# Performance work log

Hardware: AMD Instinct MI355X
Metric: run time of the kernel (lower is better)

The kernel has to match this reference:

```python
import jax, jax.numpy as jnp
import numpy as np

T, H, W, B = 9, 128, 128, 8  # size=[9,128,128], 8 samples in batch
N = 4194304


def _avg3(x):
    # AvgPool3d(kernel=(1,3,3), stride=1, pad=(0,1,1), count_include_pad=True)
    s = jax.lax.reduce_window(x, 0.0, jax.lax.add, (1, 1, 1, 3, 3), (1, 1, 1, 1, 1),
                              ((0, 0), (0, 0), (0, 0), (1, 1), (1, 1)))
    return s / 9.0


def _inorm(x, eps=1e-5):
    # InstanceNorm3d(affine=False): normalize over (T,H,W) per sample/channel
    m = x.mean(axis=(2, 3, 4), keepdims=True)
    v = x.var(axis=(2, 3, 4), keepdims=True)
    return (x - m) * jax.lax.rsqrt(v + eps)


def _time_corr(x):
    bx = (x > 0).astype(x.dtype)
    bx = jnp.concatenate([bx, bx[:, :, -1:]], axis=2)  # ReplicationPad3d back in T
    prev = _avg3(bx)
    around = (prev[:, :, :-1] * bx[:, :, 1:] > 4.0 / 9.0).astype(x.dtype)
    return _avg3(around)


def _dyn_conv(x, fc1_w, fc2_w, dyn_w):
    # Dynamic_Conv, kernel (3,1,1): attention over k=4 weight banks, per-sample conv
    a = x.mean(axis=(2, 3, 4))                       # [B,C] global avg pool
    a = jax.nn.relu(a @ fc1_w.T)
    a = jax.nn.softmax(a @ fc2_w.T, axis=1)          # [B,k]
    w = jnp.einsum('bk,koid->boid', a, dyn_w)        # [B,O,I,3]
    xp = jnp.pad(x, ((0, 0), (0, 0), (1, 1), (0, 0), (0, 0)))  # pad T
    t = x.shape[2]
    out = jnp.einsum('boi,bithw->bothw', w[..., 0], xp[:, :, 0:t])
    out = out + jnp.einsum('boi,bithw->bothw', w[..., 1], xp[:, :, 1:1 + t])
    out = out + jnp.einsum('boi,bithw->bothw', w[..., 2], xp[:, :, 2:2 + t])
    return out


def _voxelize(t, x, y, p, b):
    # per-batch normalize t by max, then bilinear-in-time scatter-add over T bins
    tmax = jax.ops.segment_max(t, b, num_segments=B)
    ts = (t / tmax[b]) * T                                         # [N]
    bins = jnp.arange(T, dtype=ts.dtype)
    vals = jnp.maximum(1.0 - jnp.abs(ts[None, :] - bins[:, None]), 0.0)  # [T,N]
    base = x + W * y + W * H * T * p + 2 * W * H * T * b           # [N]
    idx = base[None, :] + W * H * jnp.arange(T, dtype=base.dtype)[:, None]
    vox = jnp.zeros(B * 2 * T * H * W, dtype=ts.dtype).at[idx].add(vals)
    return vox.reshape(B, 2, T, H, W)


def setup_inputs() -> dict:
    key = jax.random.key(0)
    ks = jax.random.split(key, 10)
    t = jax.random.uniform(ks[0], (N,), dtype=jnp.float32)
    x = jax.random.randint(ks[1], (N,), 0, W, dtype=jnp.int32)
    y = jax.random.randint(ks[2], (N,), 0, H, dtype=jnp.int32)
    p = jax.random.randint(ks[3], (N,), 0, 2, dtype=jnp.int32)
    b = jnp.sort(jax.random.randint(ks[4], (N,), 0, B, dtype=jnp.int32))
    conv1_w = jax.random.normal(ks[5], (16, 2), jnp.float32) / np.sqrt(2.0)
    fc1_w = jax.random.normal(ks[6], (8, 16), jnp.float32) / np.sqrt(16.0)
    fc2_w = jax.random.normal(ks[7], (4, 8), jnp.float32) / np.sqrt(8.0)
    dyn_w = jax.random.normal(ks[8], (4, 16, 16, 3), jnp.float32) / np.sqrt(48.0)
    conv3_w = jax.random.normal(ks[9], (2, 16), jnp.float32) / np.sqrt(16.0)
    return {"t": t, "x": x, "y": y, "p": p, "b": b,
            "conv1_w": conv1_w, "fc1_w": fc1_w, "fc2_w": fc2_w,
            "dyn_w": dyn_w, "conv3_w": conv3_w}


def reference(t, x, y, p, b, conv1_w, fc1_w, fc2_w, dyn_w, conv3_w):
    vox = _voxelize(t, x, y, p, b)                     # [B,2,T,H,W]
    mask = _time_corr(vox)
    h = _inorm(vox)
    h = jnp.einsum('oc,bcthw->bothw', conv1_w, h)      # 1x1x1 conv 2->16
    h = _dyn_conv(h, fc1_w, fc2_w, dyn_w)
    h = jnp.einsum('oc,bcthw->bothw', conv3_w, h)      # 1x1x1 conv 16->2
    out = _inorm(jax.nn.sigmoid(h) * mask)
    return out
```

## Files before the change

### kernel.cpp

```cpp
#include <hip/hip_runtime.h>
#include <math.h>

#define TT 9
#define HH 128
#define WW 128
#define BB 8
#define SLICE (HH*WW)
#define CHW (TT*SLICE)
#define BCH (2*CHW)
#define TOT (BB*BCH)
#define INV_M (1.0f/147456.0f)
#define NYG 32
#define NBK (9*NYG)
#define SEGCAP 4096u
#define SSCALE 274877906944.0f
#define INV_SSCALE (1.0/274877906944.0)

__global__ void __launch_bounds__(1024) k_bounds(
        const int* __restrict__ b, int* __restrict__ start, int n,
        const float* __restrict__ conv1_w, const float* __restrict__ dyn_w,
        const float* __restrict__ conv3_w, float* __restrict__ Kc,
        unsigned* __restrict__ tailz, unsigned* __restrict__ cursor, int initCur) {
    if (blockIdx.x == 1) {
        if (threadIdx.x < 72) tailz[threadIdx.x] = 0u;
        if (initCur)
            for (int i = threadIdx.x; i < 8 * NBK; i += 1024)
                cursor[i] = (unsigned)i * SEGCAP;
        return;
    }
    int tid = threadIdx.x;
    if (tid < 9) {
        if (tid == 0) start[0] = 0;
        else if (tid == 8) start[8] = n;
        else {
            int lo = 0, hi = n;
            while (lo < hi) { int mid = (lo + hi) >> 1; if (b[mid] < tid) lo = mid + 1; else hi = mid; }
            start[tid] = lo;
        }
    }
    if (tid >= 32 && tid < 44) {
        int q = tid - 32;
        int d = q % 3, c = (q / 3) & 1, o2 = q / 6;
        float acc = 0.0f;
        for (int o = 0; o < 16; ++o) {
            float c3 = conv3_w[o2 * 16 + o];
            for (int i = 0; i < 16; ++i) {
                float wsum = 0.0f;
                for (int k = 0; k < 4; ++k) wsum += dyn_w[((k * 16 + o) * 16 + i) * 3 + d];
                acc += c3 * (0.25f * wsum) * conv1_w[i * 2 + c];
            }
        }
        Kc[q] = acc;
    }
}

__global__ void __launch_bounds__(1024) k_tmax(
        const float* __restrict__ t, const int* __restrict__ start,
        unsigned* __restrict__ gmax) {
    __shared__ unsigned sm[1024];
    int bi = blockIdx.x & 7, cj = blockIdx.x >> 3, nb = gridDim.x >> 3;
    int s = start[bi], e = start[bi + 1];
    unsigned m = 0u;
    if (e > s) {
        int a = (s + 3) & ~3; if (a > e) a = e;
        int z = e & ~3;       if (z < a) z = a;
        if (cj == 0) {
            int i = s + (int)threadIdx.x;
            if (i < a) { unsigned v = __float_as_uint(t[i]); if (v > m) m = v; }
            i = z + (int)threadIdx.x;
            if (i < e) { unsigned v = __float_as_uint(t[i]); if (v > m) m = v; }
        }
        long nq = (long)(z - a) >> 2;
        long per = (nq + nb - 1) / nb;
        long q0 = (long)cj * per; if (q0 > nq) q0 = nq;
        long q1 = q0 + per;       if (q1 > nq) q1 = nq;
        const float4* tp = (const float4*)(t + a);
        for (long i = q0 + threadIdx.x; i < q1; i += 1024) {
            float4 u = tp[i];
            unsigned c = __float_as_uint(fmaxf(fmaxf(u.x, u.y), fmaxf(u.z, u.w)));
            if (c > m) m = c;
        }
    }
    sm[threadIdx.x] = m;
    __syncthreads();
    for (int ofs = 512; ofs > 0; ofs >>= 1) {
        if (threadIdx.x < ofs && sm[threadIdx.x + ofs] > sm[threadIdx.x])
            sm[threadIdx.x] = sm[threadIdx.x + ofs];
        __syncthreads();
    }
    if (threadIdx.x == 0 && sm[0]) atomicMax(&gmax[bi], sm[0]);
}

__global__ void __launch_bounds__(1024) k_place(
        const float* __restrict__ t, const int* __restrict__ x,
        const int* __restrict__ y, const int* __restrict__ p,
        const unsigned* __restrict__ gmax, const int* __restrict__ start,
        unsigned* __restrict__ cursor, int2* __restrict__ rec) {
    __shared__ unsigned lh[NBK], lc[NBK], cbase[NBK];
    __shared__ unsigned wsum[5];
    __shared__ int2 srec[4096];
    __shared__ unsigned short sbkt[4096];
    int bi = blockIdx.x & 7, cj = blockIdx.x >> 3, nb = gridDim.x >> 3;
    int s = start[bi], e = start[bi + 1];
    if (e <= s) return;
    float tmax = __uint_as_float(gmax[bi]);
    int a = (s + 3) & ~3; if (a > e) a = e;
    int z = e & ~3;       if (z < a) z = a;
    long nq = (long)(z - a) >> 2;
    long per = (nq + nb - 1) / nb;
    long q0 = (long)cj * per; if (q0 > nq) q0 = nq;
    long q1 = q0 + per;       if (q1 > nq) q1 = nq;
    const float4* tp = (const float4*)(t + a);
    const int4*   xp = (const int4*)(x + a);
    const int4*   yp = (const int4*)(y + a);
    const int4*   pp = (const int4*)(p + a);
    for (long base = q0; base < q1; base += 1024) {
        if (threadIdx.x < NBK) lh[threadIdx.x] = 0u;
        __syncthreads();
        long qi = base + threadIdx.x;
        int lb[4]; float tsv[4]; int keyv[4]; unsigned rank[4];
        #pragma unroll
        for (int k = 0; k < 4; ++k) lb[k] = -1;
        if (qi < q1) {
            float4 tv = tp[qi]; int4 xv = xp[qi]; int4 yv = yp[qi]; int4 pv = pp[qi];
            float tq[4] = {tv.x, tv.y, tv.z, tv.w};
            int   xq[4] = {xv.x, xv.y, xv.z, xv.w};
            int   yq[4] = {yv.x, yv.y, yv.z, yv.w};
            int   pq[4] = {pv.x, pv.y, pv.z, pv.w};
            #pragma unroll
            for (int k = 0; k < 4; ++k) {
                float ts = tq[k] / tmax * 9.0f;
                int i0 = (int)floorf(ts);
                if ((unsigned)i0 < 9u) {
                    lb[k] = i0 * NYG + (yq[k] >> 2);
                    tsv[k] = ts;
                    keyv[k] = xq[k] + (yq[k] << 7) + (pq[k] << 14);
                }
            }
        }
        #pragma unroll
        for (int k = 0; k < 4; ++k)
            if (lb[k] >= 0) rank[k] = atomicAdd(&lh[lb[k]], 1u);
        __syncthreads();
        unsigned v = 0, inc = 0;
        if (threadIdx.x < 320) {
            v = (threadIdx.x < NBK) ? lh[threadIdx.x] : 0u;
            inc = v;
            #pragma unroll
            for (int ofs = 1; ofs < 64; ofs <<= 1) {
                unsigned u = __shfl_up(inc, ofs, 64);
                if ((threadIdx.x & 63) >= ofs) inc += u;
            }
            if ((threadIdx.x & 63) == 63) wsum[threadIdx.x >> 6] = inc;
        }
        __syncthreads();
        if (threadIdx.x < NBK) {
            unsigned ex = inc - v;
            int w = threadIdx.x >> 6;
            for (int j = 0; j < w; ++j) ex += wsum[j];
            cbase[threadIdx.x] = ex;
            lc[threadIdx.x] = v ? atomicAdd(&cursor[bi * NBK + threadIdx.x], v) : 0u;
        }
        __syncthreads();
        #pragma unroll
        for (int k = 0; k < 4; ++k)
            if (lb[k] >= 0) {
                unsigned sl_ = cbase[lb[k]] + rank[k];
                srec[sl_] = make_int2(__float_as_int(tsv[k]), keyv[k]);
                sbkt[sl_] = (unsigned short)lb[k];
            }
        __syncthreads();
        unsigned tot = cbase[NBK - 1] + lh[NBK - 1];
        #pragma unroll
        for (int h = 0; h < 4; ++h) {
            unsigned slot = threadIdx.x + h * 1024;
            if (slot < tot) {
                int bkt = sbkt[slot];
                unsigned dst = lc[bkt] + (slot - cbase[bkt]);
                if (dst < (unsigned)(bi * NBK + bkt + 1) * SEGCAP)
                    rec[dst] = srec[slot];
            }
        }
        __syncthreads();
    }
    if (cj == 0) {
        int i = -1;
        if ((int)threadIdx.x < a - s) i = s + threadIdx.x;
        else if (threadIdx.x >= 64 && (int)(threadIdx.x - 64) < e - z) i = z + (threadIdx.x - 64);
        if (i >= 0) {
            float ts = t[i] / tmax * 9.0f;
            int i0 = (int)floorf(ts);
            if ((unsigned)i0 < 9u) {
                int lbx = i0 * NYG + (y[i] >> 2);
                unsigned slot = atomicAdd(&cursor[bi * NBK + lbx], 1u);
                if (slot < (unsigned)(bi * NBK + lbx + 1) * SEGCAP)
                    rec[slot] = make_int2(__float_as_int(ts), x[i] + (y[i] << 7) + (p[i] << 14));
            }
        }
    }
}

#define CELL(K) (((K) & 511) | (((K) >> 5) & 512))
#define DEP1(TSB, KEY) { float ts_ = __int_as_float(TSB); \
    unsigned long long sq_ = (unsigned long long)(ts_ * SSCALE); \
    atomicAdd(&asl[CELL(KEY)], (1ull << 48) | sq_); }

__global__ void __launch_bounds__(1024) k_accum9(
        const int2* __restrict__ rec, const unsigned* __restrict__ cursor,
        float* __restrict__ vox, float* __restrict__ s1) {
    __shared__ unsigned long long asl[1024];
    __shared__ float rs[1024], rq[1024];
    int bb = blockIdx.x, yg = blockIdx.y;
    int cell = threadIdx.x;
    int pch = cell >> 9, row = (cell >> 7) & 3, xx = cell & 127;
    float* vp = vox + (size_t)bb * BCH + (size_t)pch * CHW
              + (size_t)(((yg << 2) + row) << 7) + xx;
    double Cp = 0.0, Sp = 0.0;
    float ls = 0.f, lq = 0.f;
    for (int t = 0; t < 9; ++t) {
        asl[cell] = 0ull;
        __syncthreads();
        int lb = bb * NBK + t * NYG + yg;
        unsigned s = (unsigned)lb * SEGCAP;
        unsigned e = cursor[lb];
        unsigned cap = s + SEGCAP; if (e > cap) e = cap;
        unsigned a = (s + 1) & ~1u, z = e & ~1u; if (z < a) z = a;
        if (threadIdx.x == 0 && s < a && s < e) { int2 r = rec[s]; DEP1(r.x, r.y) }
        if (threadIdx.x == 1 && z < e)          { int2 r = rec[z]; DEP1(r.x, r.y) }
        int n2 = (int)((z - a) >> 1);
        const int4* rp = (const int4*)(rec + a);
        for (int i = threadIdx.x; i < n2; i += 1024) {
            int4 q = rp[i];
            DEP1(q.x, q.y)
            DEP1(q.z, q.w)
        }
        __syncthreads();
        unsigned long long Av = asl[cell];
        double C = (double)(unsigned)(Av >> 48);
        double S = (double)(Av & 0xFFFFFFFFFFFFull) * INV_SSCALE;
        float v = (float)(C * (double)(1 + t) - S + (Sp - Cp * (double)(t - 1)));
        vp[t * SLICE] = v;
        ls += v; lq += v * v;
        Cp = C; Sp = S;
        __syncthreads();
    }
    rs[threadIdx.x] = ls; rq[threadIdx.x] = lq;
    __syncthreads();
    for (int ofs = 256; ofs > 0; ofs >>= 1) {
        if ((threadIdx.x & 511) < ofs) {
            rs[threadIdx.x] += rs[threadIdx.x + ofs];
            rq[threadIdx.x] += rq[threadIdx.x + ofs];
        }
        __syncthreads();
    }
    if (threadIdx.x == 0)   { atomicAdd(&s1[bb * 2],     rs[0]);   atomicAdd(&s1[16 + bb * 2],     rq[0]); }
    if (threadIdx.x == 512) { atomicAdd(&s1[bb * 2 + 1], rs[512]); atomicAdd(&s1[16 + bb * 2 + 1], rq[512]); }
}

__global__ void __launch_bounds__(1024, 4) k_scat(
        const float* __restrict__ t, const int* __restrict__ x,
        const int* __restrict__ y, const int* __restrict__ p,
        const unsigned* __restrict__ gmax, const int* __restrict__ start,
        float* __restrict__ vox) {
    __shared__ float sl[2 * SLICE];
    int tg = blockIdx.x, bb = blockIdx.y;
    int cs = start[bb], ce = start[bb + 1];
    for (int j = threadIdx.x; j < 2 * SLICE; j += 1024) sl[j] = 0.0f;
    __syncthreads();
    float tmax = __uint_as_float(gmax[bb]);
    float ftg = (float)tg;
    for (int i = cs + threadIdx.x; i < ce; i += 1024) {
        float ts = t[i] / tmax * 9.0f;
        float fl = floorf(ts);
        int i0 = (int)fl;
        bool h0 = (i0 == tg), h1 = (i0 + 1 == tg);
        if (h0 | h1) {
            float w = h0 ? (1.0f - (ts - fl)) : (1.0f - (ftg - ts));
            int hw = x[i] + (y[i] << 7) + (p[i] << 14);
            atomicAdd(&sl[hw], w);
        }
    }
    __syncthreads();
    float* dst = vox + (size_t)bb * BCH + (size_t)tg * SLICE;
    for (int j = threadIdx.x; j < SLICE; j += 1024) {
        dst[j]       = sl[j];
        dst[CHW + j] = sl[SLICE + j];
    }
}

__global__ void k_stats1(const float* __restrict__ vox, float* __restrict__ s1) {
    __shared__ float ss[256], sq[256];
    int bc = blockIdx.x >> 5, part = blockIdx.x & 31;
    const float4* vp = (const float4*)(vox + (long)bc * CHW);
    const int per = (CHW / 4) / 32;
    float s = 0.f, q = 0.f;
    for (int j = part * per + threadIdx.x; j < (part + 1) * per; j += 256) {
        float4 v = vp[j];
        s += v.x + v.y + v.z + v.w;
        q += v.x * v.x + v.y * v.y + v.z * v.z + v.w * v.w;
    }
    ss[threadIdx.x] = s; sq[threadIdx.x] = q;
    __syncthreads();
    for (int ofs = 128; ofs > 0; ofs >>= 1) {
        if (threadIdx.x < ofs) { ss[threadIdx.x] += ss[threadIdx.x + ofs]; sq[threadIdx.x] += sq[threadIdx.x + ofs]; }
        __syncthreads();
    }
    if (threadIdx.x == 0) { atomicAdd(&s1[bc], ss[0]); atomicAdd(&s1[16 + bc], sq[0]); }
}

#define STRIP 32
__global__ void k_mask(const float* __restrict__ vox, float* __restrict__ mask) {
    __shared__ unsigned char sbx[36 * 128];
    __shared__ unsigned char sar[34 * 128];
    int bid = blockIdx.x;
    int strip = bid & 3;
    int t = (bid >> 2) % 9;
    int c = (bid / 36) & 1;
    int bb = bid / 72;
    long off = (long)bb * BCH + (long)c * CHW;
    const float* vt = vox + off + (long)t * SLICE;
    int tn = (t + 1 < 9) ? t + 1 : 8;
    const float* vn = vox + off + (long)tn * SLICE;
    int y0 = strip * STRIP;
    for (int j = threadIdx.x; j < 36 * 128; j += 256) {
        int r = j >> 7, xx = j & 127;
        int gy = y0 - 2 + r;
        sbx[j] = ((unsigned)gy < 128u && vt[(gy << 7) + xx] > 0.0f) ? 1 : 0;
    }
    __syncthreads();
    for (int j = threadIdx.x; j < 34 * 128; j += 256) {
        int ra = j >> 7, xx = j & 127;
        int gy = y0 - 1 + ra;
        unsigned char v = 0;
        if ((unsigned)gy < 128u) {
            int s = 0;
            for (int rs = ra; rs <= ra + 2; ++rs)
                for (int dx = -1; dx <= 1; ++dx) {
                    int x2 = xx + dx; if ((unsigned)x2 >= 128u) continue;
                    s += sbx[(rs << 7) + x2];
                }
            v = (vn[(gy << 7) + xx] > 0.0f && s >= 5) ? 1 : 0;
        }
        sar[j] = v;
    }
    __syncthreads();
    float* mt = mask + off + (long)t * SLICE;
    for (int j = threadIdx.x; j < STRIP * 128; j += 256) {
        int q = j >> 7, xx = j & 127;
        int s = 0;
        for (int ra = q; ra <= q + 2; ++ra)
            for (int dx = -1; dx <= 1; ++dx) {
                int x2 = xx + dx; if ((unsigned)x2 >= 128u) continue;
                s += sar[(ra << 7) + x2];
            }
        mt[((y0 + q) << 7) + xx] = (float)s / 9.0f;
    }
}

__global__ void __launch_bounds__(256) k_g(
        const float* __restrict__ vox, float* __restrict__ gm,
        const float* __restrict__ s1, const float* __restrict__ Kc,
        float* __restrict__ s2) {
    __shared__ float snrm[32];
    if (threadIdx.x < 16) {
        float mm = s1[threadIdx.x] * INV_M;
        float var = s1[16 + threadIdx.x] * INV_M - mm * mm;
        float inv = rsqrtf(var + 1e-5f);
        snrm[threadIdx.x] = inv;
        snrm[16 + threadIdx.x] = -mm * inv;
    }
    __syncthreads();
    int idx = blockIdx.x * 256 + threadIdx.x;
    int hw = idx & (SLICE - 1);
    int o2 = (idx >> 14) & 1;
    int bb = idx >> 15;
    const float* v0 = vox + (size_t)bb * BCH + hw;
    const float* v1 = v0 + CHW;
    float* go = gm + (size_t)bb * BCH + (size_t)o2 * CHW + hw;
    float a[9], d[9], m[9];
    #pragma unroll
    for (int tt = 0; tt < 9; ++tt) a[tt] = v0[tt * SLICE];
    #pragma unroll
    for (int tt = 0; tt < 9; ++tt) d[tt] = v1[tt * SLICE];
    #pragma unroll
    for (int tt = 0; tt < 9; ++tt) m[tt] = go[tt * SLICE];
    float sc0 = snrm[bb * 2], sh0 = snrm[16 + bb * 2];
    float sc1 = snrm[bb * 2 + 1], sh1 = snrm[16 + bb * 2 + 1];
    float k00 = Kc[o2 * 6 + 0], k01 = Kc[o2 * 6 + 1], k02 = Kc[o2 * 6 + 2];
    float k10 = Kc[o2 * 6 + 3], k11 = Kc[o2 * 6 + 4], k12 = Kc[o2 * 6 + 5];
    #pragma unroll
    for (int tt = 0; tt < 9; ++tt) { a[tt] = a[tt] * sc0 + sh0; d[tt] = d[tt] * sc1 + sh1; }
    float ls = 0.f, lq = 0.f;
    #pragma unroll
    for (int tt = 0; tt < 9; ++tt) {
        float pre = k01 * a[tt] + k11 * d[tt];
        if (tt > 0) pre += k00 * a[tt - 1] + k10 * d[tt - 1];
        if (tt < 8) pre += k02 * a[tt + 1] + k12 * d[tt + 1];
        float sig = 1.0f / (1.0f + expf(-pre));
        float g = sig * m[tt];
        go[tt * SLICE] = g;
        ls += g; lq += g * g;
    }
    __shared__ float ss[256], sq[256];
    ss[threadIdx.x] = ls; sq[threadIdx.x] = lq;
    __syncthreads();
    for (int ofs = 128; ofs > 0; ofs >>= 1) {
        if (threadIdx.x < ofs) { ss[threadIdx.x] += ss[threadIdx.x + ofs]; sq[threadIdx.x] += sq[threadIdx.x + ofs]; }
        __syncthreads();
    }
    if (threadIdx.x == 0) {
        int bc = bb * 2 + o2;
        atomicAdd(&s2[bc], ss[0]); atomicAdd(&s2[16 + bc], sq[0]);
    }
}

__global__ void k_norm(float* __restrict__ out, const float* __restrict__ s2) {
    int i4 = blockIdx.x * 256 + threadIdx.x;
    int bc = i4 / (CHW / 4);
    float m = s2[bc] * INV_M;
    float var = s2[16 + bc] * INV_M - m * m;
    float inv = rsqrtf(var + 1e-5f);
    float4 v = ((float4*)out)[i4];
    v.x = (v.x - m) * inv; v.y = (v.y - m) * inv;
    v.z = (v.z - m) * inv; v.w = (v.w - m) * inv;
    ((float4*)out)[i4] = v;
}

extern "C" void kernel_launch(void* const* d_in, const int* in_sizes, int n_in,
                              void* d_out, int out_size, void* d_ws, size_t ws_size,
                              hipStream_t stream) {
    const float* t  = (const float*)d_in[0];
    const int*   x  = (const int*)d_in[1];
    const int*   y  = (const int*)d_in[2];
    const int*   p  = (const int*)d_in[3];
    const int*   b  = (const int*)d_in[4];
    const float* conv1_w = (const float*)d_in[5];
    const float* dyn_w   = (const float*)d_in[8];
    const float* conv3_w = (const float*)d_in[9];
    float* out = (float*)d_out;
    int n = in_sizes[0];

    const long RECF = 2L * 8 * NBK * SEGCAP;
    long availF = (long)(ws_size / sizeof(float));
    long need = (long)TOT + RECF + 8192;
    int useBuckets = (availF >= need);

    float* ws   = (float*)d_ws;
    float* vox  = ws;
    int2*  rec  = (int2*)(ws + TOT);
    float* tail = ws + TOT + (useBuckets ? RECF : 0);
    unsigned* gmax    = (unsigned*)tail;
    float*    s1      = tail + 8;
    float*    s2      = tail + 40;
    float*    Kc      = tail + 72;
    int*      start   = (int*)(tail + 84);
    unsigned* cursor  = (unsigned*)(tail + 96);

    k_bounds<<<2, 1024, 0, stream>>>(b, start, n, conv1_w, dyn_w, conv3_w, Kc,
                                     (unsigned*)tail, cursor, useBuckets);
    k_tmax<<<256, 1024, 0, stream>>>(t, start, gmax);
    if (useBuckets) {
        k_place<<<512, 1024, 0, stream>>>(t, x, y, p, gmax, start, cursor, rec);
        k_accum9<<<dim3(8, NYG), 1024, 0, stream>>>(rec, cursor, vox, s1);
    } else {
        k_scat<<<dim3(9, 8, 1), 1024, 0, stream>>>(t, x, y, p, gmax, start, vox);
        k_stats1<<<512, 256, 0, stream>>>(vox, s1);
    }
    k_mask<<<576, 256, 0, stream>>>(vox, out);
    k_g<<<1024, 256, 0, stream>>>(vox, out, s1, Kc, s2);
    k_norm<<<TOT / 1024, 256, 0, stream>>>(out, s2);
}
```

Before: 125.9 us.

## Fuse time-correlation mask into sigmoid/gate kernel with per-tile shared memory

Merges the separate mask kernel into the gating kernel. Each block handles one batch, channel and an 8-row strip across all 9 time steps, computes the binarized mask and both 3x3 box filters in shared memory, then applies the mask to the sigmoid output. This avoids writing the mask to global memory and reading it back, and removes one launch. In exchange only 256 blocks run, each with serialized per-time-step syncs and halo rows reloaded from vox, which may cost parallelism.

Result: slower. 135.7 us (+7.7%).

```diff
diff --git a/kernel.cpp b/kernel.cpp
--- a/kernel.cpp
+++ b/kernel.cpp
@@ -308,60 +308,17 @@
     if (threadIdx.x == 0) { atomicAdd(&s1[bc], ss[0]); atomicAdd(&s1[16 + bc], sq[0]); }
 }
 
-#define STRIP 32
-__global__ void k_mask(const float* __restrict__ vox, float* __restrict__ mask) {
-    __shared__ unsigned char sbx[36 * 128];
-    __shared__ unsigned char sar[34 * 128];
-    int bid = blockIdx.x;
-    int strip = bid & 3;
-    int t = (bid >> 2) % 9;
-    int c = (bid / 36) & 1;
-    int bb = bid / 72;
-    long off = (long)bb * BCH + (long)c * CHW;
-    const float* vt = vox + off + (long)t * SLICE;
-    int tn = (t + 1 < 9) ? t + 1 : 8;
-    const float* vn = vox + off + (long)tn * SLICE;
-    int y0 = strip * STRIP;
-    for (int j = threadIdx.x; j < 36 * 128; j += 256) {
-        int r = j >> 7, xx = j & 127;
-        int gy = y0 - 2 + r;
-        sbx[j] = ((unsigned)gy < 128u && vt[(gy << 7) + xx] > 0.0f) ? 1 : 0;
-    }
-    __syncthreads();
-    for (int j = threadIdx.x; j < 34 * 128; j += 256) {
-        int ra = j >> 7, xx = j & 127;
-        int gy = y0 - 1 + ra;
-        unsigned char v = 0;
-        if ((unsigned)gy < 128u) {
-            int s = 0;
-            for (int rs = ra; rs <= ra + 2; ++rs)
-                for (int dx = -1; dx <= 1; ++dx) {
-                    int x2 = xx + dx; if ((unsigned)x2 >= 128u) continue;
-                    s += sbx[(rs << 7) + x2];
-                }
-            v = (vn[(gy << 7) + xx] > 0.0f && s >= 5) ? 1 : 0;
-        }
-        sar[j] = v;
-    }
-    __syncthreads();
-    float* mt = mask + off + (long)t * SLICE;
-    for (int j = threadIdx.x; j < STRIP * 128; j += 256) {
-        int q = j >> 7, xx = j & 127;
-        int s = 0;
-        for (int ra = q; ra <= q + 2; ++ra)
-            for (int dx = -1; dx <= 1; ++dx) {
-                int x2 = xx + dx; if ((unsigned)x2 >= 128u) continue;
-                s += sar[(ra << 7) + x2];
-            }
-        mt[((y0 + q) << 7) + xx] = (float)s / 9.0f;
-    }
-}
-
-__global__ void __launch_bounds__(256) k_g(
-        const float* __restrict__ vox, float* __restrict__ gm,
+__global__ void __launch_bounds__(256) k_mg(
+        const float* __restrict__ vox, float* __restrict__ out,
         const float* __restrict__ s1, const float* __restrict__ Kc,
         float* __restrict__ s2) {
     __shared__ float snrm[32];
+    __shared__ unsigned char sbx[9][12][128];
+    __shared__ unsigned char sar[10][128];
+    __shared__ unsigned char marr[9][8][128];
+    __shared__ float red[256], red2[256];
+    int bb = blockIdx.x, o2 = blockIdx.y, yg = blockIdx.z;
+    int y0 = yg << 3;
     if (threadIdx.x < 16) {
         float mm = s1[threadIdx.x] * INV_M;
         float var = s1[16 + threadIdx.x] * INV_M - mm * mm;
@@ -369,48 +326,82 @@
         snrm[threadIdx.x] = inv;
         snrm[16 + threadIdx.x] = -mm * inv;
     }
-    __syncthreads();
-    int idx = blockIdx.x * 256 + threadIdx.x;
-    int hw = idx & (SLICE - 1);
-    int o2 = (idx >> 14) & 1;
-    int bb = idx >> 15;
-    const float* v0 = vox + (size_t)bb * BCH + hw;
-    const float* v1 = v0 + CHW;
-    float* go = gm + (size_t)bb * BCH + (size_t)o2 * CHW + hw;
-    float a[9], d[9], m[9];
-    #pragma unroll
-    for (int tt = 0; tt < 9; ++tt) a[tt] = v0[tt * SLICE];
-    #pragma unroll
-    for (int tt = 0; tt < 9; ++tt) d[tt] = v1[tt * SLICE];
-    #pragma unroll
-    for (int tt = 0; tt < 9; ++tt) m[tt] = go[tt * SLICE];
+    const float* vb = vox + (size_t)bb * BCH + (size_t)o2 * CHW;
+    for (int j = threadIdx.x; j < 9 * 12 * 128; j += 256) {
+        int xx = j & 127, r = (j >> 7) % 12, tt = j / (12 * 128);
+        int gy = y0 - 2 + r;
+        sbx[tt][r][xx] = ((unsigned)gy < 128u &&
+                          vb[tt * SLICE + (gy << 7) + xx] > 0.0f) ? 1 : 0;
+    }
+    __syncthreads();
+    for (int tt = 0; tt < 9; ++tt) {
+        int tn = (tt + 1 < 9) ? tt + 1 : 8;
+        for (int j = threadIdx.x; j < 10 * 128; j += 256) {
+            int xx = j & 127, ra = j >> 7;
+            int gy = y0 - 1 + ra;
+            unsigned char v = 0;
+            if ((unsigned)gy < 128u) {
+                int s = 0;
+                for (int rs = ra; rs <= ra + 2; ++rs)
+                    for (int dx = -1; dx <= 1; ++dx) {
+                        int x2 = xx + dx; if ((unsigned)x2 >= 128u) continue;
+                        s += sbx[tt][rs][x2];
+                    }
+                v = (sbx[tn][ra + 1][xx] && s >= 5) ? 1 : 0;
+            }
+            sar[ra][xx] = v;
+        }
+        __syncthreads();
+        for (int j = threadIdx.x; j < 8 * 128; j += 256) {
+            int xx = j & 127, q = j >> 7;
+            int s = 0;
+            for (int ra = q; ra <= q + 2; ++ra)
+                for (int dx = -1; dx <= 1; ++dx) {
+                    int x2 = xx + dx; if ((unsigned)x2 >= 128u) continue;
+                    s += sar[ra][x2];
+                }
+            marr[tt][q][xx] = (unsigned char)s;
+        }
+        __syncthreads();
+    }
     float sc0 = snrm[bb * 2], sh0 = snrm[16 + bb * 2];
     float sc1 = snrm[bb * 2 + 1], sh1 = snrm[16 + bb * 2 + 1];
     float k00 = Kc[o2 * 6 + 0], k01 = Kc[o2 * 6 + 1], k02 = Kc[o2 * 6 + 2];
     float k10 = Kc[o2 * 6 + 3], k11 = Kc[o2 * 6 + 4], k12 = Kc[o2 * 6 + 5];
-    #pragma unroll
-    for (int tt = 0; tt < 9; ++tt) { a[tt] = a[tt] * sc0 + sh0; d[tt] = d[tt] * sc1 + sh1; }
+    const float* v0 = vox + (size_t)bb * BCH;
+    const float* v1 = v0 + CHW;
+    float* go = out + (size_t)bb * BCH + (size_t)o2 * CHW;
     float ls = 0.f, lq = 0.f;
     #pragma unroll
-    for (int tt = 0; tt < 9; ++tt) {
-        float pre = k01 * a[tt] + k11 * d[tt];
-        if (tt > 0) pre += k00 * a[tt - 1] + k10 * d[tt - 1];
-        if (tt < 8) pre += k02 * a[tt + 1] + k12 * d[tt + 1];
-        float sig = 1.0f / (1.0f + expf(-pre));
-        float g = sig * m[tt];
-        go[tt * SLICE] = g;
-        ls += g; lq += g * g;
-    }
-    __shared__ float ss[256], sq[256];
-    ss[threadIdx.x] = ls; sq[threadIdx.x] = lq;
+    for (int k = 0; k < 4; ++k) {
+        int j = threadIdx.x + (k << 8);
+        int q = j >> 7, xx = j & 127;
+        int hw = ((y0 + q) << 7) + xx;
+        float a[9], d[9];
+        #pragma unroll
+        for (int tt = 0; tt < 9; ++tt) a[tt] = v0[tt * SLICE + hw] * sc0 + sh0;
+        #pragma unroll
+        for (int tt = 0; tt < 9; ++tt) d[tt] = v1[tt * SLICE + hw] * sc1 + sh1;
+        #pragma unroll
+        for (int tt = 0; tt < 9; ++tt) {
+            float pre = k01 * a[tt] + k11 * d[tt];
+            if (tt > 0) pre += k00 * a[tt - 1] + k10 * d[tt - 1];
+            if (tt < 8) pre += k02 * a[tt + 1] + k12 * d[tt + 1];
+            float sig = 1.0f / (1.0f + expf(-pre));
+            float g = sig * ((float)marr[tt][q][xx] / 9.0f);
+            go[tt * SLICE + hw] = g;
+            ls += g; lq += g * g;
+        }
+    }
+    red[threadIdx.x] = ls; red2[threadIdx.x] = lq;
     __syncthreads();
     for (int ofs = 128; ofs > 0; ofs >>= 1) {
-        if (threadIdx.x < ofs) { ss[threadIdx.x] += ss[threadIdx.x + ofs]; sq[threadIdx.x] += sq[threadIdx.x + ofs]; }
+        if (threadIdx.x < ofs) { red[threadIdx.x] += red[threadIdx.x + ofs]; red2[threadIdx.x] += red2[threadIdx.x + ofs]; }
         __syncthreads();
     }
     if (threadIdx.x == 0) {
         int bc = bb * 2 + o2;
-        atomicAdd(&s2[bc], ss[0]); atomicAdd(&s2[16 + bc], sq[0]);
+        atomicAdd(&s2[bc], red[0]); atomicAdd(&s2[16 + bc], red2[0]);
     }
 }
 
@@ -466,7 +457,6 @@
         k_scat<<<dim3(9, 8, 1), 1024, 0, stream>>>(t, x, y, p, gmax, start, vox);
         k_stats1<<<512, 256, 0, stream>>>(vox, s1);
     }
-    k_mask<<<576, 256, 0, stream>>>(vox, out);
-    k_g<<<1024, 256, 0, stream>>>(vox, out, s1, Kc, s2);
+    k_mg<<<dim3(8, 2, 16), 256, 0, stream>>>(vox, out, s1, Kc, s2);
     k_norm<<<TOT / 1024, 256, 0, stream>>>(out, s2);
 }
```
